# Kernel optimization log

Hardware: AMD Instinct MI355X
Metric: run time of the kernel (lower is better)

The kernel has to match this reference:

```python
import jax, jax.numpy as jnp
import numpy as np

D_MODEL = 256
N_HEADS = 8
EPS = 1e-6


def _split_heads(x, h=N_HEADS):
    # (b, n, D) -> (b, h, n, d)
    b, n, D = x.shape
    return x.reshape(b, n, h, D // h).transpose(0, 2, 1, 3)


def _merge_heads(x):
    # (b, h, n, d) -> (b, n, D)
    b, h, n, d = x.shape
    return x.transpose(0, 2, 1, 3).reshape(b, n, h * d)


def _hodge_diag(x, q, k, inv):
    # diagonal discrete Hodge operator: per-position scalar from q.k
    d = q.shape[-1]
    hval = jnp.einsum('bhmd,bhmd->bhm', q, k) / jnp.sqrt(jnp.asarray(d, x.dtype))
    if inv:
        hval = 1.0 / (hval + EPS)
    return hval[..., None] * x


def _forward(x_v, x_e, x_f, d_0, d_1,
             W_vq, W_vk, W_eq, W_ek, W_einvq, W_einvk, W_ev, W_fq, W_fk, W_o):
    # project + split into heads: (b, h, n, d_head)
    v_Q = _split_heads(x_v @ W_vq)
    v_K = _split_heads(x_v @ W_vk)
    e_Q = _split_heads(x_e @ W_eq)
    e_K = _split_heads(x_e @ W_ek)
    e_inv_Q = _split_heads(x_e @ W_einvq)
    e_inv_K = _split_heads(x_e @ W_einvk)
    e_V = _split_heads(x_e @ W_ev)
    f_Q = _split_heads(x_f @ W_fq)
    f_K = _split_heads(x_f @ W_fk)

    # --- up-Laplacian branch: *1^{-1} d_1^T *2 d_1 ---
    _x = e_V
    _x = jnp.einsum('bkm,bhmd->bhkd', d_1, _x)          # d_1 @ x   (edges -> faces)
    _x = _hodge_diag(_x, f_Q, f_K, inv=False)            # *2
    _x = jnp.einsum('bkm,bhkd->bhmd', d_1, _x)           # d_1^T @ x (faces -> edges)
    _x = _hodge_diag(_x, e_inv_Q, e_inv_K, inv=False)    # *1^{-1} (as diag ops, inv=False)

    # --- down-Laplacian branch: d_0 *0^{-1} d_0^T *1 ---
    _y = _hodge_diag(e_V, e_Q, e_K, inv=False)           # *1
    _y = jnp.einsum('bmn,bhmd->bhnd', d_0, _y)           # d_0^T @ y (edges -> vertices)
    _y = _hodge_diag(_y, v_Q, v_K, inv=True)             # *0^{-1} (reciprocal)
    _y = jnp.einsum('bmn,bhnd->bhmd', d_0, _y)           # d_0 @ y  (vertices -> edges)

    out = _merge_heads(_y + _x)                          # (b, m, D)
    return out @ W_o


def setup_inputs() -> dict:
    key = jax.random.key(0)
    ks = jax.random.split(key, 16)
    b, n, m, k, D = 2, 2048, 6144, 4096, D_MODEL
    s = 1.0 / np.sqrt(D)
    inp = {
        'x_v': jax.random.normal(ks[0], (b, n, D), jnp.float32),
        'x_e': jax.random.normal(ks[1], (b, m, D), jnp.float32),
        'x_f': jax.random.normal(ks[2], (b, k, D), jnp.float32),
        'd_0': jax.random.normal(ks[3], (b, m, n), jnp.float32) * 0.02,
        'd_1': jax.random.normal(ks[4], (b, k, m), jnp.float32) * 0.02,
    }
    names = ['W_vq', 'W_vk', 'W_eq', 'W_ek', 'W_einvq', 'W_einvk', 'W_ev', 'W_fq', 'W_fk', 'W_o']
    for i, nm in enumerate(names):
        inp[nm] = jax.random.normal(ks[5 + i], (D, D), jnp.float32) * s
    return inp


def reference(x_v, x_e, x_f, d_0, d_1,
              W_vq, W_vk, W_eq, W_ek, W_einvq, W_einvk, W_ev, W_fq, W_fk, W_o):
    return _forward(x_v, x_e, x_f, d_0, d_1,
                    W_vq, W_vk, W_eq, W_ek, W_einvq, W_einvk, W_ev, W_fq, W_fk, W_o)
```

## Files before the change

### kernel.cpp

```cpp
#include <hip/hip_runtime.h>
#include <hip/hip_bf16.h>
#include <cstdint>
#include <cstddef>


typedef __attribute__((ext_vector_type(4))) float f32x4;
typedef __attribute__((ext_vector_type(2))) unsigned short u16x2;
typedef __attribute__((ext_vector_type(4))) unsigned short u16x4;
typedef __attribute__((ext_vector_type(8))) unsigned short u16x8;
typedef __attribute__((ext_vector_type(8))) __bf16 bf16x8;

static __device__ __forceinline__ unsigned short f2bf(float f) {
  uint32_t u = __builtin_bit_cast(uint32_t, f);
  uint32_t r = (u + 0x7FFFu + ((u >> 16) & 1u)) >> 16;
  return (unsigned short)r;
}
static __device__ __forceinline__ float bf2f(unsigned short h) {
  return __builtin_bit_cast(float, (uint32_t)h << 16);
}
static __device__ __forceinline__ void st4(unsigned short* p, u16x4 v) {
  *(u16x2*)p = u16x2{v[0], v[1]};
  *(u16x2*)(p + 2) = u16x2{v[2], v[3]};
}

struct GJob {
  const unsigned short* Ah; const float* Af;
  const unsigned short* Bh; const float* Bf;
  float* C; unsigned short* C16;
  int K, ldA, ldB, S, gx, gy;
  long long sA, sB, sC;
};

template <int MODE, bool XFAST, bool BF16C>
static __device__ void gemm_body(char* smem, const GJob& J, int b) {
  const int per = J.gx * J.gy;
  const int z = b / per;
  const int wid = b - z * per;
  const int batch = z / J.S, split = z - batch * J.S;
  const unsigned short* Ah = nullptr; const float* Af = nullptr;
  const unsigned short* Bh = nullptr; const float* Bf = nullptr;
  if constexpr (MODE == 1) Af = J.Af + (long long)batch * J.sA;
  else                     Ah = J.Ah + (long long)batch * J.sA;
  if constexpr (MODE == 2) Bf = J.Bf + (long long)batch * J.sB;
  else                     Bh = J.Bh + (long long)batch * J.sB;

  const int nwg = per;
  const int q = nwg >> 3, r = nwg & 7;
  const int xcd = wid & 7, posn = wid >> 3;
  const int swz = (xcd < r ? xcd * (q + 1) : r * (q + 1) + (xcd - r) * q) + posn;
  int mt, nt;
  if constexpr (XFAST) { mt = swz % J.gx; nt = swz / J.gx; }
  else                 { mt = swz / J.gy; nt = swz - mt * J.gy; }
  const int m0 = mt * 128, n0 = nt * 128;
  const int NC = J.gy << 7;
  const int kLen = J.K / J.S, k0base = split * kLen;

  typedef unsigned short ldsrow[128][40];
  ldsrow* lds = (ldsrow*)smem;

  const int t = threadIdx.x;
  const int w4 = t >> 6, lane = t & 63;
  const int wr = w4 >> 1, wc = w4 & 1;
  const int lr = lane & 15, kq = lane >> 4;
  const int rowV = t >> 2, c8V = (t & 3) * 8;
  const int rowA8 = t >> 3, qdA = (t & 7) * 4;

  u16x8 rAh[2], rBh[2];
  f32x4 rF[4];

  auto LOAD = [&](int kb) {
    if constexpr (MODE == 1) {
      #pragma unroll
      for (int a = 0; a < 4; ++a)
        rF[a] = *(const f32x4*)(Af + (size_t)(m0 + rowA8 + 32 * a) * J.ldA + kb + qdA);
    } else {
      #pragma unroll
      for (int a = 0; a < 2; ++a)
        rAh[a] = *(const u16x8*)(Ah + (size_t)(m0 + rowV + 64 * a) * J.ldA + kb + c8V);
    }
    if constexpr (MODE == 2) {
      #pragma unroll
      for (int a = 0; a < 4; ++a)
        rF[a] = *(const f32x4*)(Bf + (size_t)(n0 + rowA8 + 32 * a) * J.ldB + kb + qdA);
    } else {
      #pragma unroll
      for (int a = 0; a < 2; ++a)
        rBh[a] = *(const u16x8*)(Bh + (size_t)(n0 + rowV + 64 * a) * J.ldB + kb + c8V);
    }
  };
  auto STORE = [&]() {
    if constexpr (MODE == 1) {
      #pragma unroll
      for (int a = 0; a < 4; ++a) {
        f32x4 v = rF[a];
        u16x4 h = {f2bf(v[0]), f2bf(v[1]), f2bf(v[2]), f2bf(v[3])};
        *(u16x4*)&lds[0][rowA8 + 32 * a][qdA] = h;
      }
    } else {
      #pragma unroll
      for (int a = 0; a < 2; ++a) *(u16x8*)&lds[0][rowV + 64 * a][c8V] = rAh[a];
    }
    if constexpr (MODE == 2) {
      #pragma unroll
      for (int a = 0; a < 4; ++a) {
        f32x4 v = rF[a];
        u16x4 h = {f2bf(v[0]), f2bf(v[1]), f2bf(v[2]), f2bf(v[3])};
        *(u16x4*)&lds[1][rowA8 + 32 * a][qdA] = h;
      }
    } else {
      #pragma unroll
      for (int a = 0; a < 2; ++a) *(u16x8*)&lds[1][rowV + 64 * a][c8V] = rBh[a];
    }
  };

  f32x4 acc[4][4] = {};
  LOAD(k0base);
  for (int kk = 0; kk < kLen; kk += 32) {
    STORE();
    __syncthreads();
    if (kk + 32 < kLen) LOAD(k0base + kk + 32);

    bf16x8 ah[4], bh[4];
    #pragma unroll
    for (int i = 0; i < 4; ++i) {
      ah[i] = __builtin_bit_cast(bf16x8, *(const u16x8*)&lds[0][wr * 64 + i * 16 + lr][kq * 8]);
      bh[i] = __builtin_bit_cast(bf16x8, *(const u16x8*)&lds[1][wc * 64 + i * 16 + lr][kq * 8]);
    }
    #pragma unroll
    for (int i = 0; i < 4; ++i)
      #pragma unroll
      for (int j = 0; j < 4; ++j)
        acc[i][j] = __builtin_amdgcn_mfma_f32_16x16x32_bf16(ah[i], bh[j], acc[i][j], 0, 0, 0);
    __syncthreads();
  }

  if constexpr (BF16C) {
    unsigned short* C16 = J.C16 + (long long)z * J.sC;
    #pragma unroll
    for (int i = 0; i < 4; ++i)
      #pragma unroll
      for (int j = 0; j < 4; ++j) {
        unsigned short* cp = C16 + (size_t)(m0 + wr * 64 + i * 16 + kq * 4) * NC + n0 + wc * 64 + j * 16 + lr;
        #pragma unroll
        for (int qq = 0; qq < 4; ++qq) cp[(size_t)qq * NC] = f2bf(acc[i][j][qq]);
      }
  } else {
    float* C = J.C + (long long)z * J.sC;
    #pragma unroll
    for (int i = 0; i < 4; ++i)
      #pragma unroll
      for (int j = 0; j < 4; ++j) {
        float* cp = C + (size_t)(m0 + wr * 64 + i * 16 + kq * 4) * NC + n0 + wc * 64 + j * 16 + lr;
        #pragma unroll
        for (int qq = 0; qq < 4; ++qq) cp[(size_t)qq * NC] = acc[i][j][qq];
      }
  }
}

template <int M0, int M1, bool XFAST, bool BF16C>
__global__ __launch_bounds__(256) void gemm_dual(GJob j0, GJob j1, int nb0) {
  __shared__ __align__(16) unsigned short lds[2][128][40];
  if ((int)blockIdx.x < nb0) gemm_body<M0, XFAST, BF16C>((char*)lds, j0, blockIdx.x);
  else                       gemm_body<M1, XFAST, BF16C>((char*)lds, j1, blockIdx.x - nb0);
}

template <bool SPLIT>
static __device__ void proj_body(char* smem, int wid, int gx, int gy,
                                 const float* __restrict__ Af,
                                 const unsigned short* __restrict__ Bh,
                                 const unsigned short* __restrict__ Bl,
                                 float* __restrict__ C) {
  const int nwg = gx * gy;
  const int q = nwg >> 3, r = nwg & 7;
  const int xcd = wid & 7, posn = wid >> 3;
  const int swz = (xcd < r ? xcd * (q + 1) : r * (q + 1) + (xcd - r) * q) + posn;
  const int mt = swz / gy;
  const int m0 = mt * 128, n0 = (swz - mt * gy) * 128;
  const int NC = gy << 7;

  typedef unsigned short ldsrow[128][40];
  ldsrow* lds = (ldsrow*)smem;

  const int t = threadIdx.x;
  const int w4 = t >> 6, lane = t & 63;
  const int wr = w4 >> 1, wc = w4 & 1;
  const int lr = lane & 15, kq = lane >> 4;
  const int rowA8 = t >> 3, qdA = (t & 7) * 4;
  const int rowV = t >> 2, c8V = (t & 3) * 8;

  f32x4 rAf[4];
  u16x8 rBh[2], rBl[2];

  auto LOAD = [&](int kb) {
    #pragma unroll
    for (int a = 0; a < 4; ++a)
      rAf[a] = *(const f32x4*)(Af + (size_t)(m0 + rowA8 + 32 * a) * 256 + kb + qdA);
    #pragma unroll
    for (int a = 0; a < 2; ++a) {
      rBh[a] = *(const u16x8*)(Bh + (size_t)(n0 + rowV + 64 * a) * 256 + kb + c8V);
      if constexpr (SPLIT)
        rBl[a] = *(const u16x8*)(Bl + (size_t)(n0 + rowV + 64 * a) * 256 + kb + c8V);
    }
  };
  auto STORE = [&]() {
    #pragma unroll
    for (int a = 0; a < 4; ++a) {
      f32x4 v = rAf[a];
      u16x4 h = {f2bf(v[0]), f2bf(v[1]), f2bf(v[2]), f2bf(v[3])};
      *(u16x4*)&lds[0][rowA8 + 32 * a][qdA] = h;
      if constexpr (SPLIT) {
        u16x4 l = {f2bf(v[0] - bf2f(h[0])), f2bf(v[1] - bf2f(h[1])),
                   f2bf(v[2] - bf2f(h[2])), f2bf(v[3] - bf2f(h[3]))};
        *(u16x4*)&lds[2][rowA8 + 32 * a][qdA] = l;
      }
    }
    #pragma unroll
    for (int a = 0; a < 2; ++a) {
      *(u16x8*)&lds[1][rowV + 64 * a][c8V] = rBh[a];
      if constexpr (SPLIT) *(u16x8*)&lds[3][rowV + 64 * a][c8V] = rBl[a];
    }
  };

  f32x4 acc[4][4] = {};
  LOAD(0);
  for (int kk = 0; kk < 256; kk += 32) {
    STORE();
    __syncthreads();
    if (kk + 32 < 256) LOAD(kk + 32);

    bf16x8 ah[4], bh[4], al[4], bl[4];
    #pragma unroll
    for (int i = 0; i < 4; ++i) {
      ah[i] = __builtin_bit_cast(bf16x8, *(const u16x8*)&lds[0][wr * 64 + i * 16 + lr][kq * 8]);
      bh[i] = __builtin_bit_cast(bf16x8, *(const u16x8*)&lds[1][wc * 64 + i * 16 + lr][kq * 8]);
      if constexpr (SPLIT) {
        al[i] = __builtin_bit_cast(bf16x8, *(const u16x8*)&lds[2][wr * 64 + i * 16 + lr][kq * 8]);
        bl[i] = __builtin_bit_cast(bf16x8, *(const u16x8*)&lds[3][wc * 64 + i * 16 + lr][kq * 8]);
      }
    }
    #pragma unroll
    for (int i = 0; i < 4; ++i)
      #pragma unroll
      for (int j = 0; j < 4; ++j) {
        acc[i][j] = __builtin_amdgcn_mfma_f32_16x16x32_bf16(ah[i], bh[j], acc[i][j], 0, 0, 0);
        if constexpr (SPLIT) {
          acc[i][j] = __builtin_amdgcn_mfma_f32_16x16x32_bf16(ah[i], bl[j], acc[i][j], 0, 0, 0);
          acc[i][j] = __builtin_amdgcn_mfma_f32_16x16x32_bf16(al[i], bh[j], acc[i][j], 0, 0, 0);
        }
      }
    __syncthreads();
  }

  #pragma unroll
  for (int i = 0; i < 4; ++i)
    #pragma unroll
    for (int j = 0; j < 4; ++j) {
      float* cp = C + (size_t)(m0 + wr * 64 + i * 16 + kq * 4) * NC + n0 + wc * 64 + j * 16 + lr;
      #pragma unroll
      for (int qq = 0; qq < 4; ++qq) cp[(size_t)qq * NC] = acc[i][j][qq];
    }
}

__global__ __launch_bounds__(256) void proj_dual(
    const float* __restrict__ xe, const unsigned short* __restrict__ W5h,
    const unsigned short* __restrict__ W5l, float* __restrict__ P1,
    const float* __restrict__ xf, const unsigned short* __restrict__ W3h,
    float* __restrict__ P3) {
  __shared__ __align__(16) unsigned short lds[4][128][40];
  if ((int)blockIdx.x < 960)
    proj_body<true>((char*)lds, blockIdx.x, 96, 10, xe, W5h, W5l, P1);
  else
    proj_body<false>((char*)lds, blockIdx.x - 960, 64, 4, xf, W3h, nullptr, P3);
}

__global__ __launch_bounds__(256) void gemm_out(
    const unsigned short* __restrict__ T2p, const unsigned short* __restrict__ T4p,
    const float* __restrict__ hEi, const unsigned short* __restrict__ Bh,
    const unsigned short* __restrict__ Bl, float* __restrict__ C) {
  const int gx = gridDim.x, gy = gridDim.y;
  const int nwg = gx * gy;
  const int wid = blockIdx.x + gx * blockIdx.y;
  const int q = nwg >> 3, r = nwg & 7;
  const int xcd = wid & 7, posn = wid >> 3;
  const int swz = (xcd < r ? xcd * (q + 1) : r * (q + 1) + (xcd - r) * q) + posn;
  const int mt = swz / gy;
  const int m0 = mt * 128, n0 = (swz - mt * gy) * 128;

  __shared__ unsigned short lds[4][128][40];
  const int t = threadIdx.x;
  const int w4 = t >> 6, lane = t & 63;
  const int wr = w4 >> 1, wc = w4 & 1;
  const int lr = lane & 15, kq = lane >> 4;
  const long long slab = 6144LL * 256;

  f32x4 acc[4][4] = {};

  for (int kb = 0; kb < 256; kb += 32) {
    #pragma unroll
    for (int a = 0; a < 4; ++a) {
      int idx = t + 256 * a;
      int row = idx >> 3, qd = (idx & 7) * 4;
      int rg = m0 + row;
      int b = rg >= 6144;
      int pos = rg - b * 6144;
      int ck = kb + qd;
      float s = hEi[((size_t)b * 8 + (ck >> 5)) * 6144 + pos];
      const unsigned short* b2 = T2p + ((long long)(b * 2) * 6144 + pos) * 256 + ck;
      const unsigned short* b4 = T4p + ((long long)(b * 2) * 6144 + pos) * 256 + ck;
      u16x4 p20 = *(const u16x4*)b2, p21 = *(const u16x4*)(b2 + slab);
      u16x4 p40 = *(const u16x4*)b4, p41 = *(const u16x4*)(b4 + slab);
      f32x4 t2 = {bf2f(p20[0]) + bf2f(p21[0]), bf2f(p20[1]) + bf2f(p21[1]),
                  bf2f(p20[2]) + bf2f(p21[2]), bf2f(p20[3]) + bf2f(p21[3])};
      f32x4 t4 = {bf2f(p40[0]) + bf2f(p41[0]), bf2f(p40[1]) + bf2f(p41[1]),
                  bf2f(p40[2]) + bf2f(p41[2]), bf2f(p40[3]) + bf2f(p41[3])};
      f32x4 v = t4 + t2 * s;
      u16x4 h = {f2bf(v[0]), f2bf(v[1]), f2bf(v[2]), f2bf(v[3])};
      *(u16x4*)&lds[0][row][qd] = h;
      u16x4 l = {f2bf(v[0] - bf2f(h[0])), f2bf(v[1] - bf2f(h[1])),
                 f2bf(v[2] - bf2f(h[2])), f2bf(v[3] - bf2f(h[3]))};
      *(u16x4*)&lds[2][row][qd] = l;
    }
    #pragma unroll
    for (int a = 0; a < 2; ++a) {
      int idx = t + 256 * a;
      int row = idx >> 2, c8 = (idx & 3) * 8;
      *(u16x8*)&lds[1][row][c8] = *(const u16x8*)(Bh + (size_t)(n0 + row) * 256 + kb + c8);
      *(u16x8*)&lds[3][row][c8] = *(const u16x8*)(Bl + (size_t)(n0 + row) * 256 + kb + c8);
    }
    __syncthreads();

    bf16x8 ah[4], bh[4], al[4], bl[4];
    #pragma unroll
    for (int i = 0; i < 4; ++i) {
      ah[i] = __builtin_bit_cast(bf16x8, *(const u16x8*)&lds[0][wr * 64 + i * 16 + lr][kq * 8]);
      bh[i] = __builtin_bit_cast(bf16x8, *(const u16x8*)&lds[1][wc * 64 + i * 16 + lr][kq * 8]);
      al[i] = __builtin_bit_cast(bf16x8, *(const u16x8*)&lds[2][wr * 64 + i * 16 + lr][kq * 8]);
      bl[i] = __builtin_bit_cast(bf16x8, *(const u16x8*)&lds[3][wc * 64 + i * 16 + lr][kq * 8]);
    }
    #pragma unroll
    for (int i = 0; i < 4; ++i)
      #pragma unroll
      for (int j = 0; j < 4; ++j) {
        acc[i][j] = __builtin_amdgcn_mfma_f32_16x16x32_bf16(ah[i], bh[j], acc[i][j], 0, 0, 0);
        acc[i][j] = __builtin_amdgcn_mfma_f32_16x16x32_bf16(ah[i], bl[j], acc[i][j], 0, 0, 0);
        acc[i][j] = __builtin_amdgcn_mfma_f32_16x16x32_bf16(al[i], bh[j], acc[i][j], 0, 0, 0);
      }
    __syncthreads();
  }

  #pragma unroll
  for (int i = 0; i < 4; ++i)
    #pragma unroll
    for (int j = 0; j < 4; ++j) {
      float* cp = C + (size_t)(m0 + wr * 64 + i * 16 + kq * 4) * 256 + n0 + wc * 64 + j * 16 + lr;
      #pragma unroll
      for (int qq = 0; qq < 4; ++qq) cp[(size_t)qq * 256] = acc[i][j][qq];
    }
}

struct WTab {
  const float* s[8];
  unsigned short* h[8];
  unsigned short* l[8];
};
__global__ __launch_bounds__(256) void wxpose(WTab tab) {
  __shared__ __align__(16) unsigned short smem[2 * 64 * 74];
  unsigned short* thi = smem;
  unsigned short* tlo = smem + 64 * 74;
  const int idx = blockIdx.x;
  const int w = idx >> 4;
  const int r0 = (idx & 3) * 64, c0 = ((idx >> 2) & 3) * 64;
  const float* src = tab.s[w];
  unsigned short* oh = tab.h[w];
  unsigned short* ol = tab.l[w];
  const int t = threadIdx.x;
  #pragma unroll
  for (int a = 0; a < 4; ++a) {
    int idx2 = t + 256 * a;
    int tr = idx2 >> 4, tc = (idx2 & 15) * 4;
    f32x4 v = *(const f32x4*)(src + (size_t)(r0 + tr) * 256 + c0 + tc);
    u16x4 hh = {f2bf(v[0]), f2bf(v[1]), f2bf(v[2]), f2bf(v[3])};
    st4(&thi[tr * 74 + tc], hh);
    if (ol) {
      u16x4 ll = {f2bf(v[0] - bf2f(hh[0])), f2bf(v[1] - bf2f(hh[1])),
                  f2bf(v[2] - bf2f(hh[2])), f2bf(v[3] - bf2f(hh[3]))};
      st4(&tlo[tr * 74 + tc], ll);
    }
  }
  __syncthreads();
  #pragma unroll
  for (int a = 0; a < 2; ++a) {
    int idx2 = t + 256 * a;
    int orow = idx2 >> 3, oc = (idx2 & 7) * 8;
    u16x8 vh;
    #pragma unroll
    for (int j = 0; j < 8; ++j) vh[j] = thi[(oc + j) * 74 + orow];
    *(u16x8*)(oh + (size_t)(c0 + orow) * 256 + r0 + oc) = vh;
    if (ol) {
      u16x8 vl;
      #pragma unroll
      for (int j = 0; j < 8; ++j) vl[j] = tlo[(oc + j) * 74 + orow];
      *(u16x8*)(ol + (size_t)(c0 + orow) * 256 + r0 + oc) = vl;
    }
  }
}

struct PrepArgs {
  const float* d1; unsigned short* d1T;
  const float* d0; unsigned short* d0T_hi;
  const float* xv; const float* Wvq; const float* Wvk; float* hvV;
};

__global__ __launch_bounds__(256) void prep2(PrepArgs A) {
  __shared__ __align__(16) char smem[24576];
  const int t = threadIdx.x;
  const int bid = blockIdx.x;

  if (bid < 512) {
    float* sx = (float*)smem;
    float* sq = (float*)(smem + 8192);
    float* sk = (float*)(smem + 16384);
    const int r0 = bid * 8;
    const int j = t;
    #pragma unroll
    for (int r = 0; r < 8; ++r) sx[r * 256 + j] = A.xv[(size_t)(r0 + r) * 256 + j];
    __syncthreads();
    float qa[8] = {}, ka[8] = {};
    for (int i = 0; i < 256; ++i) {
      float wq = A.Wvq[i * 256 + j], wk = A.Wvk[i * 256 + j];
      #pragma unroll
      for (int r = 0; r < 8; ++r) {
        qa[r] = __fmaf_rn(sx[r * 256 + i], wq, qa[r]);
        ka[r] = __fmaf_rn(sx[r * 256 + i], wk, ka[r]);
      }
    }
    #pragma unroll
    for (int r = 0; r < 8; ++r) { sq[r * 256 + j] = qa[r]; sk[r * 256 + j] = ka[r]; }
    __syncthreads();
    if (j < 64) {
      const int r = j >> 3, head = j & 7;
      const float* qq = &sq[r * 256 + head * 32];
      const float* kk = &sk[r * 256 + head * 32];
      float s0 = 0.0f, s1 = 0.0f, s2 = 0.0f, s3 = 0.0f;
      #pragma unroll 1
      for (int d = 0; d < 32; d += 4) {
        s0 = __fadd_rn(s0, __fmul_rn(qq[d + 0], kk[d + 0]));
        s1 = __fadd_rn(s1, __fmul_rn(qq[d + 1], kk[d + 1]));
        s2 = __fadd_rn(s2, __fmul_rn(qq[d + 2], kk[d + 2]));
        s3 = __fadd_rn(s3, __fmul_rn(qq[d + 3], kk[d + 3]));
      }
      float p = __fadd_rn(__fadd_rn(s0, s2), __fadd_rn(s1, s3));
      float hval = __fdiv_rn(p, sqrtf(32.0f));
      float inv = __fdiv_rn(1.0f, __fadd_rn(hval, 1e-6f));
      const int row = r0 + r;
      const int b = row / 2048, pos = row - b * 2048;
      A.hvV[((size_t)b * 8 + head) * 2048 + pos] = inv;
    }
  } else if (bid < 6656) {
    const int idx = bid - 512;
    const int x = idx % 96;
    const int rem = idx / 96;
    const int y = rem & 31;
    const int b = rem >> 5;
    const int r0 = x * 64, c0 = y * 64;
    unsigned short* tile = (unsigned short*)smem;
    #pragma unroll
    for (int a = 0; a < 4; ++a) {
      int idx2 = t + 256 * a;
      int tr = idx2 >> 4, tc = (idx2 & 15) * 4;
      size_t off = ((size_t)b * 6144 + r0 + tr) * 2048 + c0 + tc;
      f32x4 v = *(const f32x4*)(A.d0 + off);
      u16x4 hh = {f2bf(v[0]), f2bf(v[1]), f2bf(v[2]), f2bf(v[3])};
      st4(&tile[tr * 74 + tc], hh);
    }
    __syncthreads();
    #pragma unroll
    for (int a = 0; a < 2; ++a) {
      int idx2 = t + 256 * a;
      int orow = idx2 >> 3, oc = (idx2 & 7) * 8;
      u16x8 vh;
      #pragma unroll
      for (int j = 0; j < 8; ++j) vh[j] = tile[(oc + j) * 74 + orow];
      *(u16x8*)(A.d0T_hi + ((size_t)b * 2048 + c0 + orow) * 6144 + r0 + oc) = vh;
    }
  } else {
    const int idx = bid - 6656;
    const int x = idx & 63;
    const int rem = idx >> 6;
    const int y = rem % 96;
    const int b = rem / 96;
    const int r0 = x * 64, c0 = y * 64;
    unsigned short* tile = (unsigned short*)smem;
    #pragma unroll
    for (int a = 0; a < 4; ++a) {
      int idx2 = t + 256 * a;
      int tr = idx2 >> 4, tc = (idx2 & 15) * 4;
      size_t off = ((size_t)b * 4096 + r0 + tr) * 6144 + c0 + tc;
      f32x4 v = *(const f32x4*)(A.d1 + off);
      u16x4 hh = {f2bf(v[0]), f2bf(v[1]), f2bf(v[2]), f2bf(v[3])};
      st4(&tile[tr * 74 + tc], hh);
    }
    __syncthreads();
    #pragma unroll
    for (int a = 0; a < 2; ++a) {
      int idx2 = t + 256 * a;
      int orow = idx2 >> 3, oc = (idx2 & 7) * 8;
      u16x8 vh;
      #pragma unroll
      for (int j = 0; j < 8; ++j) vh[j] = tile[(oc + j) * 74 + orow];
      *(u16x8*)(A.d1T + ((size_t)b * 6144 + c0 + orow) * 4096 + r0 + oc) = vh;
    }
  }
}

__global__ __launch_bounds__(256) void xpose_ev(
    const float* __restrict__ P1, unsigned short* __restrict__ eVT,
    unsigned short* __restrict__ yhi, const float* __restrict__ hE) {
  __shared__ __align__(16) unsigned short smem[2 * 64 * 74];
  unsigned short* te = smem;
  unsigned short* th = smem + 64 * 74;
  const int b = blockIdx.z;
  const int r0 = blockIdx.x * 64, c0 = blockIdx.y * 64;
  const int t = threadIdx.x;
  #pragma unroll
  for (int a = 0; a < 4; ++a) {
    int idx = t + 256 * a;
    int tr = idx >> 4, tc = (idx & 15) * 4;
    f32x4 v = *(const f32x4*)(P1 + ((size_t)b * 6144 + r0 + tr) * 1280 + 512 + c0 + tc);
    u16x4 eh = {f2bf(v[0]), f2bf(v[1]), f2bf(v[2]), f2bf(v[3])};
    st4(&te[tr * 74 + tc], eh);
    float s = hE[((size_t)b * 8 + ((c0 + tc) >> 5)) * 6144 + r0 + tr];
    f32x4 y = v * s;
    u16x4 hh = {f2bf(y[0]), f2bf(y[1]), f2bf(y[2]), f2bf(y[3])};
    st4(&th[tr * 74 + tc], hh);
  }
  __syncthreads();
  #pragma unroll
  for (int a = 0; a < 2; ++a) {
    int idx = t + 256 * a;
    int orow = idx >> 3, oc = (idx & 7) * 8;
    u16x8 ve, vh;
    #pragma unroll
    for (int j = 0; j < 8; ++j) {
      ve[j] = te[(oc + j) * 74 + orow];
      vh[j] = th[(oc + j) * 74 + orow];
    }
    size_t o = ((size_t)b * 256 + c0 + orow) * 6144 + r0 + oc;
    *(u16x8*)(eVT + o) = ve;
    *(u16x8*)(yhi + o) = vh;
  }
}

static __device__ __forceinline__ void rsc_body(
    const float* in, unsigned short* out_hi, const float* h,
    int S, int R, int P, int bid, int nblk) {
  const long long qP = P >> 2;
  const long long nq = 2LL * R * qP;
  long long i = (long long)bid * 256 + threadIdx.x;
  const long long stride = (long long)nblk * 256;
  for (; i < nq; i += stride) {
    long long b = i / (R * qP);
    long long rem = i - b * (R * qP);
    int row = (int)(rem / qP);
    long long qc = rem - (long long)row * qP;
    const f32x4* base = (const f32x4*)in + ((b * S) * R + row) * qP + qc;
    f32x4 v = base[0];
    for (int s = 1; s < S; ++s) v += base[(long long)s * R * qP];
    v *= *(const f32x4*)(h + ((size_t)b * 8 + (row >> 5)) * P + (qc << 2));
    u16x4 hh = {f2bf(v[0]), f2bf(v[1]), f2bf(v[2]), f2bf(v[3])};
    ((u16x4*)out_hi)[i] = hh;
  }
}

__global__ void rsc2(const float* in1, unsigned short* o1h, const float* hF,
                     const float* in3, unsigned short* o3h, const float* hV) {
  if (blockIdx.x < 2048)
    rsc_body(in1, o1h, hF, 3, 256, 4096, blockIdx.x, 2048);
  else
    rsc_body(in3, o3h, hV, 6, 256, 2048, blockIdx.x - 2048, 1024);
}

__global__ __launch_bounds__(256) void dots(
    const float* __restrict__ P1, float* __restrict__ hE, float* __restrict__ hEi,
    const float* __restrict__ P3, float* __restrict__ hF) {
  const int wv = threadIdx.x >> 6, lane = threadIdx.x & 63;
  if (blockIdx.x < 3072) {
    const int row = blockIdx.x * 4 + wv;
    const float* base = P1 + (size_t)row * 1280 + lane * 4;
    f32x4 qv = *(const f32x4*)(base);
    f32x4 kv = *(const f32x4*)(base + 256);
    float p = qv[0] * kv[0] + qv[1] * kv[1] + qv[2] * kv[2] + qv[3] * kv[3];
    p += __shfl_xor(p, 1); p += __shfl_xor(p, 2); p += __shfl_xor(p, 4);
    f32x4 q2 = *(const f32x4*)(base + 768);
    f32x4 k2 = *(const f32x4*)(base + 1024);
    float p2 = q2[0] * k2[0] + q2[1] * k2[1] + q2[2] * k2[2] + q2[3] * k2[3];
    p2 += __shfl_xor(p2, 1); p2 += __shfl_xor(p2, 2); p2 += __shfl_xor(p2, 4);
    if ((lane & 7) == 0) {
      const int head = lane >> 3;
      const int b = row / 6144, pos = row % 6144;
      hE[((size_t)b * 8 + head) * 6144 + pos] = p * 0.17677669529663687f;
      hEi[((size_t)b * 8 + head) * 6144 + pos] = p2 * 0.17677669529663687f;
    }
  } else {
    const int row = (blockIdx.x - 3072) * 4 + wv;
    const float* base = P3 + (size_t)row * 512 + lane * 4;
    f32x4 qv = *(const f32x4*)(base);
    f32x4 kv = *(const f32x4*)(base + 256);
    float p = qv[0] * kv[0] + qv[1] * kv[1] + qv[2] * kv[2] + qv[3] * kv[3];
    p += __shfl_xor(p, 1); p += __shfl_xor(p, 2); p += __shfl_xor(p, 4);
    if ((lane & 7) == 0) {
      const int head = lane >> 3;
      const int b = row / 4096, pos = row % 4096;
      hF[((size_t)b * 8 + head) * 4096 + pos] = p * 0.17677669529663687f;
    }
  }
}

extern "C" void kernel_launch(void* const* d_in, const int* in_sizes, int n_in,
                              void* d_out, int out_size, void* d_ws, size_t ws_size,
                              hipStream_t stream) {
  const float* x_v = (const float*)d_in[0];
  const float* x_e = (const float*)d_in[1];
  const float* x_f = (const float*)d_in[2];
  const float* d0  = (const float*)d_in[3];
  const float* d1  = (const float*)d_in[4];
  float* out = (float*)d_out;

  const int NV = 2048, ME = 6144, KF = 4096;

  char* ws = (char*)d_ws;
  size_t o = 0;
  auto alloc = [&](size_t bytes) { size_t r = o; o = (o + bytes + 255) & ~255ULL; return r; };

  unsigned short* Wcat5_hi = (unsigned short*)(ws + alloc(1280 * 256 * 2));
  unsigned short* Wcat5_lo = (unsigned short*)(ws + alloc(1280 * 256 * 2));
  unsigned short* W3_hi = (unsigned short*)(ws + alloc(512 * 256 * 2));
  unsigned short* Wo_hi = (unsigned short*)(ws + alloc(256 * 256 * 2));
  unsigned short* Wo_lo = (unsigned short*)(ws + alloc(256 * 256 * 2));
  float* pHvE  = (float*)(ws + alloc(2 * 8 * ME * 4));
  float* pHvEi = (float*)(ws + alloc(2 * 8 * ME * 4));
  float* pHvF  = (float*)(ws + alloc(2 * 8 * KF * 4));
  float* pHvV  = (float*)(ws + alloc(2 * 8 * NV * 4));
  unsigned short* d1T_hi = (unsigned short*)(ws + alloc((size_t)2 * ME * KF * 2));
  unsigned short* d0T_hi = (unsigned short*)(ws + alloc((size_t)2 * NV * ME * 2));
  unsigned short* eVT_hi = (unsigned short*)(ws + alloc((size_t)2 * 256 * ME * 2));
  unsigned short* Y0T_hi = (unsigned short*)(ws + alloc((size_t)2 * 256 * ME * 2));
  unsigned short* T1sT_hi = (unsigned short*)(ws + alloc((size_t)2 * 256 * KF * 2));
  unsigned short* T3sT_hi = (unsigned short*)(ws + alloc((size_t)2 * 256 * NV * 2));
  float* pP1 = (float*)(ws + alloc((size_t)12288 * 1280 * 4));
  float* pP3 = (float*)(ws + alloc((size_t)8192 * 512 * 4));
  float* pTp1 = (float*)(ws + alloc((size_t)2 * 3 * 256 * KF * 4));
  float* pTp3 = (float*)(ws + alloc((size_t)2 * 6 * 256 * NV * 4));
  unsigned short* pT2p = (unsigned short*)(ws + alloc((size_t)2 * 2 * ME * 256 * 2));
  unsigned short* pT4p = (unsigned short*)(ws + alloc((size_t)2 * 2 * ME * 256 * 2));

  dim3 blk(256);

  WTab tab;
  tab.s[0] = (const float*)d_in[7];  tab.h[0] = Wcat5_hi;          tab.l[0] = Wcat5_lo;
  tab.s[1] = (const float*)d_in[8];  tab.h[1] = Wcat5_hi + 65536;  tab.l[1] = Wcat5_lo + 65536;
  tab.s[2] = (const float*)d_in[11]; tab.h[2] = Wcat5_hi + 131072; tab.l[2] = Wcat5_lo + 131072;
  tab.s[3] = (const float*)d_in[9];  tab.h[3] = Wcat5_hi + 196608; tab.l[3] = Wcat5_lo + 196608;
  tab.s[4] = (const float*)d_in[10]; tab.h[4] = Wcat5_hi + 262144; tab.l[4] = Wcat5_lo + 262144;
  tab.s[5] = (const float*)d_in[12]; tab.h[5] = W3_hi;             tab.l[5] = nullptr;
  tab.s[6] = (const float*)d_in[13]; tab.h[6] = W3_hi + 65536;     tab.l[6] = nullptr;
  tab.s[7] = (const float*)d_in[14]; tab.h[7] = Wo_hi;             tab.l[7] = Wo_lo;
  wxpose<<<128, blk, 0, stream>>>(tab);

  proj_dual<<<1216, blk, 0, stream>>>(x_e, Wcat5_hi, Wcat5_lo, pP1, x_f, W3_hi, pP3);
  dots<<<5120, blk, 0, stream>>>(pP1, pHvE, pHvEi, pP3, pHvF);
  xpose_ev<<<dim3(96, 4, 2), blk, 0, stream>>>(pP1, eVT_hi, Y0T_hi, pHvE);

  PrepArgs pa;
  pa.d1 = d1; pa.d1T = d1T_hi;
  pa.d0 = d0; pa.d0T_hi = d0T_hi;
  pa.xv = x_v; pa.Wvq = (const float*)d_in[5]; pa.Wvk = (const float*)d_in[6];
  pa.hvV = pHvV;
  prep2<<<18944, blk, 0, stream>>>(pa);

  GJob jT1 = {}, jT3 = {};
  jT1.Ah = eVT_hi; jT1.Bf = d1; jT1.C = pTp1;
  jT1.K = ME; jT1.ldA = ME; jT1.ldB = ME; jT1.S = 3; jT1.gx = 2; jT1.gy = 32;
  jT1.sA = 256LL * ME; jT1.sB = (long long)KF * ME; jT1.sC = 256LL * KF;
  jT3.Ah = Y0T_hi; jT3.Bh = d0T_hi; jT3.C = pTp3;
  jT3.K = ME; jT3.ldA = ME; jT3.ldB = ME; jT3.S = 6; jT3.gx = 2; jT3.gy = 16;
  jT3.sA = 256LL * ME; jT3.sB = (long long)NV * ME; jT3.sC = 256LL * NV;
  gemm_dual<2, 0, true, false><<<768, blk, 0, stream>>>(jT1, jT3, 384);

  rsc2<<<3072, blk, 0, stream>>>(pTp1, T1sT_hi, pHvF, pTp3, T3sT_hi, pHvV);

  GJob jT2 = {}, jT4 = {};
  jT2.Ah = d1T_hi; jT2.Bh = T1sT_hi; jT2.C16 = pT2p;
  jT2.K = KF; jT2.ldA = KF; jT2.ldB = KF; jT2.S = 2; jT2.gx = 48; jT2.gy = 2;
  jT2.sA = (long long)ME * KF; jT2.sB = 256LL * KF; jT2.sC = (long long)ME * 256;
  jT4.Af = d0; jT4.Bh = T3sT_hi; jT4.C16 = pT4p;
  jT4.K = NV; jT4.ldA = NV; jT4.ldB = NV; jT4.S = 2; jT4.gx = 48; jT4.gy = 2;
  jT4.sA = (long long)ME * NV; jT4.sB = 256LL * NV; jT4.sC = (long long)ME * 256;
  gemm_dual<0, 1, false, true><<<768, blk, 0, stream>>>(jT2, jT4, 384);

  gemm_out<<<dim3(96, 2, 1), blk, 0, stream>>>(pT2p, pT4p, pHvEi, Wo_hi, Wo_lo, out);
}
```

Measured before the change: 374.2 us.

## Co-schedule T1 GEMM with prep and overlap T1 reduction with T3 GEMM

Moves the T1 GEMM (eVT times d1) into the prep kernel as extra blocks, since it only depends on xpose_ev outputs and d1 read as fp32. The T3 GEMM is paired with the split-K reduction of T1 in one launch, and the T3 reduction gets its own kernel. The aim is to fill idle compute units and cut tail effects by overlapping independent stages across kernel boundaries. The risk is uneven block durations and shared-memory pressure in the fused kernels, and the extra launch for the separate reduction.

```diff
diff --git a/kernel.cpp b/kernel.cpp
--- a/kernel.cpp
+++ b/kernel.cpp
@@ -162,6 +162,40 @@
   __shared__ __align__(16) unsigned short lds[2][128][40];
   if ((int)blockIdx.x < nb0) gemm_body<M0, XFAST, BF16C>((char*)lds, j0, blockIdx.x);
   else                       gemm_body<M1, XFAST, BF16C>((char*)lds, j1, blockIdx.x - nb0);
+}
+
+static __device__ __forceinline__ void rsc_body(
+    const float* in, unsigned short* out_hi, const float* h,
+    int S, int R, int P, int bid, int nblk) {
+  const long long qP = P >> 2;
+  const long long nq = 2LL * R * qP;
+  long long i = (long long)bid * 256 + threadIdx.x;
+  const long long stride = (long long)nblk * 256;
+  for (; i < nq; i += stride) {
+    long long b = i / (R * qP);
+    long long rem = i - b * (R * qP);
+    int row = (int)(rem / qP);
+    long long qc = rem - (long long)row * qP;
+    const f32x4* base = (const f32x4*)in + ((b * S) * R + row) * qP + qc;
+    f32x4 v = base[0];
+    for (int s = 1; s < S; ++s) v += base[(long long)s * R * qP];
+    v *= *(const f32x4*)(h + ((size_t)b * 8 + (row >> 5)) * P + (qc << 2));
+    u16x4 hh = {f2bf(v[0]), f2bf(v[1]), f2bf(v[2]), f2bf(v[3])};
+    ((u16x4*)out_hi)[i] = hh;
+  }
+}
+
+__global__ __launch_bounds__(256) void t3_rsc1(
+    GJob jT3, const float* in1, unsigned short* o1h, const float* hF) {
+  __shared__ __align__(16) unsigned short lds[2][128][40];
+  if ((int)blockIdx.x < 384)
+    gemm_body<0, true, false>((char*)lds, jT3, blockIdx.x);
+  else
+    rsc_body(in1, o1h, hF, 3, 256, 4096, blockIdx.x - 384, 2048);
+}
+
+__global__ void rsc3k(const float* in3, unsigned short* o3h, const float* hV) {
+  rsc_body(in3, o3h, hV, 6, 256, 2048, blockIdx.x, 1024);
 }
 
 template <bool SPLIT>
@@ -411,10 +445,16 @@
   const float* xv; const float* Wvq; const float* Wvk; float* hvV;
 };
 
-__global__ __launch_bounds__(256) void prep2(PrepArgs A) {
+__global__ __launch_bounds__(256) void prep3(PrepArgs A, GJob jT1) {
   __shared__ __align__(16) char smem[24576];
   const int t = threadIdx.x;
-  const int bid = blockIdx.x;
+  int bid = blockIdx.x;
+
+  if (bid < 384) {
+    gemm_body<2, true, false>(smem, jT1, bid);
+    return;
+  }
+  bid -= 384;
 
   if (bid < 512) {
     float* sx = (float*)smem;
@@ -549,35 +589,6 @@
     *(u16x8*)(eVT + o) = ve;
     *(u16x8*)(yhi + o) = vh;
   }
-}
-
-static __device__ __forceinline__ void rsc_body(
-    const float* in, unsigned short* out_hi, const float* h,
-    int S, int R, int P, int bid, int nblk) {
-  const long long qP = P >> 2;
-  const long long nq = 2LL * R * qP;
-  long long i = (long long)bid * 256 + threadIdx.x;
-  const long long stride = (long long)nblk * 256;
-  for (; i < nq; i += stride) {
-    long long b = i / (R * qP);
-    long long rem = i - b * (R * qP);
-    int row = (int)(rem / qP);
-    long long qc = rem - (long long)row * qP;
-    const f32x4* base = (const f32x4*)in + ((b * S) * R + row) * qP + qc;
-    f32x4 v = base[0];
-    for (int s = 1; s < S; ++s) v += base[(long long)s * R * qP];
-    v *= *(const f32x4*)(h + ((size_t)b * 8 + (row >> 5)) * P + (qc << 2));
-    u16x4 hh = {f2bf(v[0]), f2bf(v[1]), f2bf(v[2]), f2bf(v[3])};
-    ((u16x4*)out_hi)[i] = hh;
-  }
-}
-
-__global__ void rsc2(const float* in1, unsigned short* o1h, const float* hF,
-                     const float* in3, unsigned short* o3h, const float* hV) {
-  if (blockIdx.x < 2048)
-    rsc_body(in1, o1h, hF, 3, 256, 4096, blockIdx.x, 2048);
-  else
-    rsc_body(in3, o3h, hV, 6, 256, 2048, blockIdx.x - 2048, 1024);
 }
 
 __global__ __launch_bounds__(256) void dots(
@@ -671,23 +682,24 @@
   dots<<<5120, blk, 0, stream>>>(pP1, pHvE, pHvEi, pP3, pHvF);
   xpose_ev<<<dim3(96, 4, 2), blk, 0, stream>>>(pP1, eVT_hi, Y0T_hi, pHvE);
 
+  GJob jT1 = {};
+  jT1.Ah = eVT_hi; jT1.Bf = d1; jT1.C = pTp1;
+  jT1.K = ME; jT1.ldA = ME; jT1.ldB = ME; jT1.S = 3; jT1.gx = 2; jT1.gy = 32;
+  jT1.sA = 256LL * ME; jT1.sB = (long long)KF * ME; jT1.sC = 256LL * KF;
   PrepArgs pa;
   pa.d1 = d1; pa.d1T = d1T_hi;
   pa.d0 = d0; pa.d0T_hi = d0T_hi;
   pa.xv = x_v; pa.Wvq = (const float*)d_in[5]; pa.Wvk = (const float*)d_in[6];
   pa.hvV = pHvV;
-  prep2<<<18944, blk, 0, stream>>>(pa);
-
-  GJob jT1 = {}, jT3 = {};
-  jT1.Ah = eVT_hi; jT1.Bf = d1; jT1.C = pTp1;
-  jT1.K = ME; jT1.ldA = ME; jT1.ldB = ME; jT1.S = 3; jT1.gx = 2; jT1.gy = 32;
-  jT1.sA = 256LL * ME; jT1.sB = (long long)KF * ME; jT1.sC = 256LL * KF;
+  prep3<<<19328, blk, 0, stream>>>(pa, jT1);
+
+  GJob jT3 = {};
   jT3.Ah = Y0T_hi; jT3.Bh = d0T_hi; jT3.C = pTp3;
   jT3.K = ME; jT3.ldA = ME; jT3.ldB = ME; jT3.S = 6; jT3.gx = 2; jT3.gy = 16;
   jT3.sA = 256LL * ME; jT3.sB = (long long)NV * ME; jT3.sC = 256LL * NV;
-  gemm_dual<2, 0, true, false><<<768, blk, 0, stream>>>(jT1, jT3, 384);
-
-  rsc2<<<3072, blk, 0, stream>>>(pTp1, T1sT_hi, pHvF, pTp3, T3sT_hi, pHvV);
+  t3_rsc1<<<2432, blk, 0, stream>>>(jT3, pTp1, T1sT_hi, pHvF);
+
+  rsc3k<<<1024, blk, 0, stream>>>(pTp3, T3sT_hi, pHvV);
 
   GJob jT2 = {}, jT4 = {};
   jT2.Ah = d1T_hi; jT2.Bh = T1sT_hi; jT2.C16 = pT2p;
```

Result: no change. 373.8 us (-0.1%).
